# Optimization experiments

Measured on AMD Instinct MI355X. Metric: run time of the kernel, lower is better.

The kernel has to match this reference:

```python
import jax, jax.numpy as jnp
import numpy as np

ROPE_BASE = 10000.0

def _rope(x, positions):
    # x: [B, H, T, hs], rotate-half (GPT-NeoX style) rotary embedding
    hs = x.shape[-1]
    half = hs // 2
    inv_freq = 1.0 / (ROPE_BASE ** (jnp.arange(half, dtype=jnp.float32) / half))
    ang = positions.astype(jnp.float32)[:, None] * inv_freq[None, :]  # [T, half]
    cos, sin = jnp.cos(ang), jnp.sin(ang)
    x1, x2 = x[..., :half], x[..., half:]
    return jnp.concatenate([x1 * cos - x2 * sin, x1 * sin + x2 * cos], axis=-1)


def setup_inputs() -> dict:
    key = jax.random.key(0)
    ks = jax.random.split(key, 8)
    B, T, OFF, C, H = 1, 1024, 1024, 2048, 16
    hs = C // H
    return {
        "x": jax.random.normal(ks[0], (B, T, C), jnp.float32),
        "cached_k": jax.random.normal(ks[1], (B, H, OFF, hs), jnp.float32),
        "cached_v": jax.random.normal(ks[2], (B, H, OFF, hs), jnp.float32),
        "W_attn": jax.random.normal(ks[3], (C, 3 * C), jnp.float32) * 0.02,
        "b_attn": jnp.zeros((3 * C,), jnp.float32),
        "W_proj": jax.random.normal(ks[4], (C, C), jnp.float32) * 0.02,
        "b_proj": jnp.zeros((C,), jnp.float32),
        "decay_raw": jax.random.normal(ks[5], (16,), jnp.float32) * 0.5,
    }


def reference(x, cached_k, cached_v, W_attn, b_attn, W_proj, b_proj, decay_raw):
    B, T, C = x.shape
    H = decay_raw.shape[0]
    hs = C // H
    off = cached_k.shape[2]

    qkv = x @ W_attn + b_attn                       # [B, T, 3C]
    q, k, v = jnp.split(qkv, 3, axis=-1)
    to_heads = lambda t: t.reshape(B, T, H, hs).transpose(0, 2, 1, 3)  # [B,H,T,hs]
    q, k, v = to_heads(q), to_heads(k), to_heads(v)

    positions = jnp.arange(off, off + T)
    q = _rope(q, positions)
    k = _rope(k, positions)

    k = jnp.concatenate([cached_k, k], axis=2)      # [B, H, T_full, hs]
    v = jnp.concatenate([cached_v, v], axis=2)
    T_full = k.shape[2]

    # causal mask over full key length, offset for cache
    neg_inf = jnp.finfo(jnp.float32).min
    q_idx = positions                               # [T]
    k_idx = jnp.arange(T_full)                      # [T_full]
    causal = jnp.where(k_idx[None, :] > q_idx[:, None], neg_inf, 0.0)  # [T, T_full]

    # per-head distance-decay log-bias
    decay = jax.nn.softplus(decay_raw)              # [H]
    dist = jnp.maximum(q_idx[:, None] - k_idx[None, :], 0).astype(jnp.float32)
    logw = -jnp.log1p(decay[:, None, None] * jnp.log1p(dist))          # [H, T, T_full]
    bias = causal[None, :, :] + logw                # [H, T, T_full]

    scale = 1.0 / jnp.sqrt(jnp.float32(hs))
    scores = jnp.einsum('bhtd,bhsd->bhts', q, k) * scale + bias[None]
    attn = jax.nn.softmax(scores, axis=-1)
    y = jnp.einsum('bhts,bhsd->bhtd', attn, v)      # [B, H, T, hs]
    y = y.transpose(0, 2, 1, 3).reshape(B, T, C)
    y = y @ W_proj + b_proj
    return (y, k, v)
```

## Files before the change

kernel.cpp:

```cpp
#include <hip/hip_runtime.h>
#include <hip/hip_bf16.h>

typedef unsigned short u16;
typedef unsigned int u32;
typedef __attribute__((ext_vector_type(4))) float f32x4;
typedef __attribute__((ext_vector_type(8))) short bf16x8;

__device__ __forceinline__ u16 f2bf(float f) {
    union { float f; u32 u; } v; v.f = f;
    return (u16)((v.u + 0x7FFFu + ((v.u >> 16) & 1u)) >> 16);
}
__device__ __forceinline__ float bf2f(u16 b) {
    union { u32 u; float f; } v; v.u = ((u32)b) << 16;
    return v.f;
}
__device__ __forceinline__ void st_out(float* p, float v) { *p = v; }
__device__ __forceinline__ void st_out(u16* p, float v) { *p = f2bf(v); }

__device__ __forceinline__ f32x4 mfma16(bf16x8 a, bf16x8 b, f32x4 c) {
    return __builtin_amdgcn_mfma_f32_16x16x32_bf16(a, b, c, 0, 0, 0);
}

#define GLD_LDS16(g, l) __builtin_amdgcn_global_load_lds( \
    (const __attribute__((address_space(1))) void*)(g),   \
    (__attribute__((address_space(3))) void*)(l), 16, 0, 0)

__global__ __launch_bounds__(256) void k_prep(
    const float* __restrict__ W_attn, const float* __restrict__ W_proj,
    const float* __restrict__ x, const float* __restrict__ decay_raw,
    u16* __restrict__ WaT, u16* __restrict__ WpT, u16* __restrict__ Xb,
    float* __restrict__ bias_tab, float* __restrict__ cosT, float* __restrict__ sinT) {
    __shared__ float tile[64][65];
    const int b = blockIdx.x, tid = threadIdx.x;
    if (b < 4096) {
        const float* src; u16* dst; int R, Cc, bx, by;
        if (b < 3072) { src = W_attn; dst = WaT; R = 2048; Cc = 6144; bx = b % 96; by = b / 96; }
        else          { src = W_proj; dst = WpT; R = 2048; Cc = 2048; bx = (b - 3072) & 31; by = (b - 3072) >> 5; }
        int c0 = bx * 64, r0 = by * 64;
#pragma unroll
        for (int it = 0; it < 16; ++it) {
            int idx = it * 256 + tid;
            int r = idx >> 6, c = idx & 63;
            tile[r][c] = src[(size_t)(r0 + r) * Cc + c0 + c];
        }
        __syncthreads();
#pragma unroll
        for (int it = 0; it < 16; ++it) {
            int idx = it * 256 + tid;
            int cc = idx >> 6, rr = idx & 63;
            dst[(size_t)(c0 + cc) * R + r0 + rr] = f2bf(tile[rr][cc]);
        }
    } else if (b < 6144) {
        int i = (b - 4096) * 256 + tid;
        float4 v = ((const float4*)x)[i];
        u32 p0 = (u32)f2bf(v.x) | ((u32)f2bf(v.y) << 16);
        u32 p1 = (u32)f2bf(v.z) | ((u32)f2bf(v.w) << 16);
        uint2 p; p.x = p0; p.y = p1;
        *(uint2*)(Xb + (size_t)i * 4) = p;
    } else {
        int i = (b - 6144) * 256 + tid;
        if (i < 16 * 2048) {
            int h = i >> 11, dist = i & 2047;
            float dec = log1pf(expf(decay_raw[h]));
            bias_tab[i] = -log1pf(dec * log1pf((float)dist));
        }
        if (i < 1024 * 64) {
            int t = i >> 6, j = i & 63;
            float inv = expf(-logf(10000.0f) * (float)j / 64.0f);
            float ang = (float)(1024 + t) * inv;
            cosT[i] = cosf(ang);
            sinT[i] = sinf(ang);
        }
    }
}

template<int BM, int BN, int WRG, int WCG, typename OT>
__global__ __launch_bounds__(256) void k_gemm_bt(
    const u16* __restrict__ A, const u16* __restrict__ Bt,
    const float* __restrict__ bias, OT* __restrict__ C,
    int M, int N, int K) {
    constexpr int BK = 64;
    constexpr int WM = BM / WRG;
    constexpr int WN = BN / WCG;
    constexpr int MR = WM / 16;
    constexpr int NR = WN / 16;
    __shared__ char lds[(BM + BN) * BK * 2];
    char* ldsA = lds;
    char* ldsB = lds + BM * BK * 2;

    const int tid = threadIdx.x;
    const int lane = tid & 63, wid = tid >> 6;
    const int wr = wid / WCG, wc = wid % WCG;
    const int lhi = lane >> 4, llo = lane & 15;
    const int m0 = blockIdx.y * BM, n0 = blockIdx.x * BN;

    f32x4 acc[MR][NR];
#pragma unroll
    for (int m = 0; m < MR; ++m)
#pragma unroll
        for (int n = 0; n < NR; ++n)
            acc[m][n] = f32x4{0.f, 0.f, 0.f, 0.f};

    for (int k0 = 0; k0 < K; k0 += BK) {
#pragma unroll
        for (int it = 0; it < (BM * 8) / 256; ++it) {
            int ci = it * 256 + wid * 64 + lane;
            int r = ci >> 3, c = ci & 7;
            int sc = c ^ (r & 7);
            GLD_LDS16(A + (size_t)(m0 + r) * K + k0 + sc * 8,
                      ldsA + (it * 256 + wid * 64) * 16);
        }
#pragma unroll
        for (int it = 0; it < (BN * 8) / 256; ++it) {
            int ci = it * 256 + wid * 64 + lane;
            int r = ci >> 3, c = ci & 7;
            int sc = c ^ (r & 7);
            GLD_LDS16(Bt + (size_t)(n0 + r) * K + k0 + sc * 8,
                      ldsB + (it * 256 + wid * 64) * 16);
        }
        __syncthreads();
#pragma unroll
        for (int kk = 0; kk < BK; kk += 32) {
            bf16x8 af[MR], bfr[NR];
            const int clb = (kk >> 3) + lhi;
#pragma unroll
            for (int m = 0; m < MR; ++m) {
                int row = wr * WM + m * 16 + llo;
                af[m] = *(const bf16x8*)(ldsA + row * 128 + ((clb ^ (row & 7)) << 4));
            }
#pragma unroll
            for (int n = 0; n < NR; ++n) {
                int row = wc * WN + n * 16 + llo;
                bfr[n] = *(const bf16x8*)(ldsB + row * 128 + ((clb ^ (row & 7)) << 4));
            }
#pragma unroll
            for (int m = 0; m < MR; ++m)
#pragma unroll
                for (int n = 0; n < NR; ++n)
                    acc[m][n] = mfma16(af[m], bfr[n], acc[m][n]);
        }
        __syncthreads();
    }
#pragma unroll
    for (int m = 0; m < MR; ++m) {
        int row = m0 + wr * WM + m * 16 + lhi * 4;
#pragma unroll
        for (int n = 0; n < NR; ++n) {
            int col = n0 + wc * WN + n * 16 + llo;
            float bv = bias[col];
#pragma unroll
            for (int j = 0; j < 4; ++j)
                st_out(&C[(size_t)(row + j) * N + col], acc[m][n][j] + bv);
        }
    }
}

__global__ void k_fuse2(const u16* __restrict__ qkv,
                        const float* __restrict__ cosT, const float* __restrict__ sinT,
                        const float* __restrict__ cached_k,
                        u16* __restrict__ qb, u16* __restrict__ kb,
                        float* __restrict__ out_k) {
    const int b = blockIdx.x;
    if (b < 4096) {
        int i = b * 256 + threadIdx.x;
        int j = i & 63;
        int t = (i >> 6) & 1023;
        int h = i >> 16;
        const u16* row = qkv + (size_t)t * 6144;
        float q1 = bf2f(row[h * 128 + j]),        q2 = bf2f(row[h * 128 + j + 64]);
        float k1 = bf2f(row[2048 + h * 128 + j]), k2 = bf2f(row[2048 + h * 128 + j + 64]);
        float cv = cosT[t * 64 + j], sv = sinT[t * 64 + j];
        float qo1 = q1 * cv - q2 * sv, qo2 = q1 * sv + q2 * cv;
        float ko1 = k1 * cv - k2 * sv, ko2 = k1 * sv + k2 * cv;
        size_t qoff = ((size_t)h * 1024 + t) * 128 + j;
        qb[qoff] = f2bf(qo1); qb[qoff + 64] = f2bf(qo2);
        size_t koff = ((size_t)h * 2048 + 1024 + t) * 128 + j;
        kb[koff] = f2bf(ko1); kb[koff + 64] = f2bf(ko2);
        out_k[koff] = ko1; out_k[koff + 64] = ko2;
    } else {
        int i = (b - 4096) * 256 + threadIdx.x;
        int d = i & 127, s = (i >> 7) & 1023, h = i >> 17;
        float v = cached_k[i];
        size_t off = ((size_t)h * 2048 + s) * 128 + d;
        out_k[off] = v;
        kb[off] = f2bf(v);
    }
}

__global__ __launch_bounds__(256) void k_v_assemble(
    const float* __restrict__ cached_v, const u16* __restrict__ qkv,
    float* __restrict__ out_v, u16* __restrict__ vt) {
    __shared__ u16 tile[64][65];
    int s0 = blockIdx.x * 64, d0 = blockIdx.y * 64, h = blockIdx.z;
    int tid = threadIdx.x;
#pragma unroll
    for (int it = 0; it < 16; ++it) {
        int idx = it * 256 + tid;
        int r = idx >> 6, c = idx & 63;
        int s = s0 + r, d = d0 + c;
        u16 v = (s < 1024)
            ? f2bf(cached_v[((size_t)h * 1024 + s) * 128 + d])
            : qkv[(size_t)(s - 1024) * 6144 + 4096 + h * 128 + d];
        tile[r][c] = v;
        out_v[((size_t)h * 2048 + s) * 128 + d] = bf2f(v);
    }
    __syncthreads();
#pragma unroll
    for (int it = 0; it < 16; ++it) {
        int idx = it * 256 + tid;
        int dd = idx >> 6, ss = idx & 63;
        vt[((size_t)h * 128 + d0 + dd) * 2048 + s0 + ss] = tile[ss][dd];
    }
}

__global__ __launch_bounds__(256, 4) void k_attn(
    const u16* __restrict__ qb,
    const u16* __restrict__ kb,
    const u16* __restrict__ vt,
    const float* __restrict__ bias_tab,
    u16* __restrict__ Pacc,
    float* __restrict__ Pm,
    float* __restrict__ Pl) {
    __shared__ char ldsK[2][32 * 256];
    __shared__ char ldsV[2][128 * 64];
    __shared__ u16 ldsP[4][16 * 36];

    const int bid = blockIdx.x;
    const int xcd = bid & 7, idx = bid >> 3;
    const int work = xcd * 128 + idx;
    const int h = work >> 6, rem = work & 63;
    const int qt = rem >> 2, chunk = rem & 3;
    const int qbase = qt * 64;
    const int tid = threadIdx.x, lane = tid & 63, wid = tid >> 6;
    const int lhi = lane >> 4, llo = lane & 15;
    const int slot = (h * 16 + qt) * 4 + chunk;

    const u16* kg = kb + (size_t)h * 2048 * 128;
    const u16* vg = vt + (size_t)h * 128 * 2048;
    const float* bt = bias_tab + h * 2048;

    bf16x8 qf[4];
    {
        const u16* qrow = qb + ((size_t)h * 1024 + qbase + wid * 16 + llo) * 128;
#pragma unroll
        for (int c = 0; c < 4; ++c)
            qf[c] = *(const bf16x8*)(qrow + c * 32 + lhi * 8);
    }

    f32x4 acc[8];
#pragma unroll
    for (int d = 0; d < 8; ++d) acc[d] = f32x4{0.f, 0.f, 0.f, 0.f};
    float mrow[4] = {-3e38f, -3e38f, -3e38f, -3e38f};
    float lrow[4] = {0.f, 0.f, 0.f, 0.f};

    const int ntiles = 34 + 2 * qt;
    const float scale = 0.08838834764831845f;
    const int qpos = 1024 + qbase + wid * 16 + lhi * 4;

    auto stage = [&](int b, int st) {
        int sbase = st * 32;
#pragma unroll
        for (int it = 0; it < 2; ++it) {
            int ci = it * 256 + tid;
            int r = ci >> 4, c = ci & 15;
            int sc = c ^ (r & 7);
            GLD_LDS16(kg + (size_t)(sbase + r) * 128 + sc * 8,
                      &ldsK[b][0] + (it * 256 + wid * 64) * 16);
        }
#pragma unroll
        for (int it = 0; it < 2; ++it) {
            int ci = it * 256 + tid;
            int r = ci >> 2, c = ci & 3;
            int sc = c ^ ((r >> 1) & 3);
            GLD_LDS16(vg + (size_t)r * 2048 + sbase + sc * 8,
                      &ldsV[b][0] + (it * 256 + wid * 64) * 16);
        }
    };

    const int st0 = chunk + 4 * ((ntiles - 1 - chunk) >> 2);
    stage(0, st0);
    __syncthreads();
    int cur = 0;
    for (int st = st0; st >= chunk; st -= 4) {
        if (st >= chunk + 4) stage(cur ^ 1, st - 4);
        const int sbase = st * 32;
        const char* lK = &ldsK[cur][0];
        const char* lV = &ldsV[cur][0];

        f32x4 sc4[2];
#pragma unroll
        for (int sub = 0; sub < 2; ++sub) {
            f32x4 s4 = f32x4{0.f, 0.f, 0.f, 0.f};
            int key = sub * 16 + llo;
#pragma unroll
            for (int c2 = 0; c2 < 4; ++c2) {
                int cl = c2 * 4 + lhi;
                bf16x8 kf = *(const bf16x8*)(lK + key * 256 + ((cl ^ (key & 7)) << 4));
                s4 = mfma16(qf[c2], kf, s4);
            }
            sc4[sub] = s4;
        }

#pragma unroll
        for (int sub = 0; sub < 2; ++sub) {
            int key = sbase + sub * 16 + llo;
#pragma unroll
            for (int j = 0; j < 4; ++j) {
                int dist = qpos + j - key;
                float bv = bt[dist < 0 ? 0 : dist];
                sc4[sub][j] = (dist < 0) ? -3e38f : sc4[sub][j] * scale + bv;
            }
        }
        float tmax[4];
        int ok = 1;
#pragma unroll
        for (int j = 0; j < 4; ++j) {
            tmax[j] = fmaxf(sc4[0][j], sc4[1][j]);
            ok &= (tmax[j] <= mrow[j] + 8.0f) ? 1 : 0;
        }
        if (!__all(ok)) {
#pragma unroll
            for (int j = 0; j < 4; ++j) {
                float t = tmax[j];
                t = fmaxf(t, __shfl_xor(t, 1));
                t = fmaxf(t, __shfl_xor(t, 2));
                t = fmaxf(t, __shfl_xor(t, 4));
                t = fmaxf(t, __shfl_xor(t, 8));
                float mnew = fmaxf(mrow[j], t);
                float fs = __expf(mrow[j] - mnew);
                mrow[j] = mnew;
                lrow[j] *= fs;
#pragma unroll
                for (int d = 0; d < 8; ++d) acc[d][j] *= fs;
            }
        }
#pragma unroll
        for (int sub = 0; sub < 2; ++sub)
#pragma unroll
            for (int j = 0; j < 4; ++j) {
                float p = __expf(sc4[sub][j] - mrow[j]);
                sc4[sub][j] = p;
                lrow[j] += p;
            }

        u16* P = &ldsP[wid][0];
#pragma unroll
        for (int sub = 0; sub < 2; ++sub)
#pragma unroll
            for (int j = 0; j < 4; ++j)
                P[(lhi * 4 + j) * 36 + sub * 16 + llo] = f2bf(sc4[sub][j]);

        bf16x8 pf = *(const bf16x8*)((const char*)P + llo * 72 + lhi * 16);
#pragma unroll
        for (int db = 0; db < 8; ++db) {
            int dr = db * 16 + llo;
            int cl = lhi ^ ((dr >> 1) & 3);
            bf16x8 vf = *(const bf16x8*)(lV + dr * 64 + cl * 16);
            acc[db] = mfma16(pf, vf, acc[db]);
        }
        __syncthreads();
        cur ^= 1;
    }

#pragma unroll
    for (int j = 0; j < 4; ++j) {
        float t = lrow[j];
        t += __shfl_xor(t, 1);
        t += __shfl_xor(t, 2);
        t += __shfl_xor(t, 4);
        t += __shfl_xor(t, 8);
        lrow[j] = t;
    }

    if (llo == 0) {
#pragma unroll
        for (int j = 0; j < 4; ++j) {
            int r = wid * 16 + lhi * 4 + j;
            Pm[(size_t)slot * 64 + r] = mrow[j];
            Pl[(size_t)slot * 64 + r] = lrow[j];
        }
    }
#pragma unroll
    for (int db = 0; db < 8; ++db)
#pragma unroll
        for (int j = 0; j < 4; ++j) {
            int r = wid * 16 + lhi * 4 + j;
            Pacc[(size_t)slot * 8192 + r * 128 + db * 16 + llo] = f2bf(acc[db][j]);
        }
}

__global__ __launch_bounds__(256) void k_merge(
    const u16* __restrict__ Pacc, const float* __restrict__ Pm,
    const float* __restrict__ Pl, u16* __restrict__ yb) {
    const int h = blockIdx.x >> 4, qt = blockIdx.x & 15;
    const int slot0 = blockIdx.x * 4;
    const int tid = threadIdx.x;
    const int r = tid >> 2, d0 = (tid & 3) * 32;

    float m[4], l[4];
#pragma unroll
    for (int c = 0; c < 4; ++c) {
        m[c] = Pm[(size_t)(slot0 + c) * 64 + r];
        l[c] = Pl[(size_t)(slot0 + c) * 64 + r];
    }
    float M = fmaxf(fmaxf(m[0], m[1]), fmaxf(m[2], m[3]));
    float w[4], L = 0.f;
#pragma unroll
    for (int c = 0; c < 4; ++c) {
        w[c] = __expf(m[c] - M);
        L += w[c] * l[c];
    }
    float inv = 1.0f / L;

    float y[32];
#pragma unroll
    for (int i = 0; i < 32; ++i) y[i] = 0.f;
#pragma unroll
    for (int c = 0; c < 4; ++c) {
        const uint4* pa = (const uint4*)(Pacc + (size_t)(slot0 + c) * 8192 + r * 128 + d0);
        float wc = w[c];
#pragma unroll
        for (int q = 0; q < 4; ++q) {
            uint4 v = pa[q];
            u32 a[4] = {v.x, v.y, v.z, v.w};
#pragma unroll
            for (int p = 0; p < 4; ++p) {
                y[q * 8 + p * 2]     += wc * bf2f((u16)(a[p] & 0xFFFF));
                y[q * 8 + p * 2 + 1] += wc * bf2f((u16)(a[p] >> 16));
            }
        }
    }
    int trow = qt * 64 + r;
    uint4 outv[4];
    u32* ow = (u32*)outv;
#pragma unroll
    for (int k = 0; k < 16; ++k)
        ow[k] = (u32)f2bf(y[2 * k] * inv) | ((u32)f2bf(y[2 * k + 1] * inv) << 16);
    uint4* dst = (uint4*)(yb + (size_t)trow * 2048 + h * 128 + d0);
#pragma unroll
    for (int q = 0; q < 4; ++q) dst[q] = outv[q];
}

extern "C" void kernel_launch(void* const* d_in, const int* in_sizes, int n_in,
                              void* d_out, int out_size, void* d_ws, size_t ws_size,
                              hipStream_t stream) {
    (void)in_sizes; (void)n_in; (void)out_size;
    const float* x         = (const float*)d_in[0];
    const float* cached_k  = (const float*)d_in[1];
    const float* cached_v  = (const float*)d_in[2];
    const float* W_attn    = (const float*)d_in[3];
    const float* b_attn    = (const float*)d_in[4];
    const float* W_proj    = (const float*)d_in[5];
    const float* b_proj    = (const float*)d_in[6];
    const float* decay_raw = (const float*)d_in[7];

    float* out_y = (float*)d_out;
    float* out_k = out_y + 2097152;
    float* out_v = out_y + 6291456;

    char* ws = (char*)d_ws;
    if (ws_size < 63569920) return;
    u16*   WaT  = (u16*)(ws);
    u16*   WpT  = (u16*)(ws + 25165824);
    u16*   Xb   = (u16*)(ws + 33554432);
    u16*   QKVb = (u16*)(ws + 37748736);
    float* BT   = (float*)(ws + 62914560);
    float* CT   = (float*)(ws + 63045632);
    float* ST   = (float*)(ws + 63307776);
    u16*   Qb   = (u16*)(ws);
    u16*   Kb   = (u16*)(ws + 4194304);
    u16*   Vt   = (u16*)(ws + 12582912);
    u16*   Yb   = (u16*)(ws + 20971520);
    float* Pm   = (float*)(ws + 33554432);
    float* Pl   = (float*)(ws + 33816576);
    u16*   Pacc = (u16*)(ws + 37748736);

    k_prep<<<6400, 256, 0, stream>>>(W_attn, W_proj, x, decay_raw, WaT, WpT, Xb, BT, CT, ST);
    k_gemm_bt<128, 96, 2, 2, u16><<<dim3(64, 8), 256, 0, stream>>>(Xb, WaT, b_attn, QKVb, 1024, 6144, 2048);
    k_fuse2<<<12288, 256, 0, stream>>>(QKVb, CT, ST, cached_k, Qb, Kb, out_k);
    k_v_assemble<<<dim3(32, 2, 16), 256, 0, stream>>>(cached_v, QKVb, out_v, Vt);
    k_attn<<<1024, 256, 0, stream>>>(Qb, Kb, Vt, BT, Pacc, Pm, Pl);
    k_merge<<<256, 256, 0, stream>>>(Pacc, Pm, Pl, Yb);
    k_gemm_bt<64, 64, 2, 2, float><<<dim3(32, 16), 256, 0, stream>>>(Yb, WpT, b_proj, out_y, 1024, 2048, 2048);
}
```

Before: 145.2 us.

## Double-buffer GEMM LDS tiles, add MFMA priority hints, split merge across more blocks

The GEMM kernel now double-buffers its LDS tiles, so the global-to-LDS load of the next K tile is issued while the current tile is being multiplied. The QKV GEMM tile shrinks from 128x96 to 128x64, which launches more blocks and offsets the doubled LDS footprint. The attention kernel wraps its MFMA sections in s_setprio so matrix work from one wave is favoured over other waves. The merge kernel splits each head/query tile across four blocks, each handling a quarter of the head dimension, giving four times the blocks with fewer registers per thread. The costs are extra LDS per block, possibly lower occupancy, and redundant m/l reads in the merge.

```diff
diff --git a/kernel.cpp b/kernel.cpp
--- a/kernel.cpp
+++ b/kernel.cpp
@@ -84,9 +84,8 @@
     constexpr int WN = BN / WCG;
     constexpr int MR = WM / 16;
     constexpr int NR = WN / 16;
-    __shared__ char lds[(BM + BN) * BK * 2];
-    char* ldsA = lds;
-    char* ldsB = lds + BM * BK * 2;
+    constexpr int LDSZ = (BM + BN) * BK * 2;
+    __shared__ char lds[2][LDSZ];
 
     const int tid = threadIdx.x;
     const int lane = tid & 63, wid = tid >> 6;
@@ -101,7 +100,9 @@
         for (int n = 0; n < NR; ++n)
             acc[m][n] = f32x4{0.f, 0.f, 0.f, 0.f};
 
-    for (int k0 = 0; k0 < K; k0 += BK) {
+    auto stage = [&](int buf, int k0) {
+        char* ldsA = &lds[buf][0];
+        char* ldsB = &lds[buf][0] + BM * BK * 2;
 #pragma unroll
         for (int it = 0; it < (BM * 8) / 256; ++it) {
             int ci = it * 256 + wid * 64 + lane;
@@ -118,7 +119,15 @@
             GLD_LDS16(Bt + (size_t)(n0 + r) * K + k0 + sc * 8,
                       ldsB + (it * 256 + wid * 64) * 16);
         }
-        __syncthreads();
+    };
+
+    stage(0, 0);
+    __syncthreads();
+    int cur = 0;
+    for (int k0 = 0; k0 < K; k0 += BK) {
+        if (k0 + BK < K) stage(cur ^ 1, k0 + BK);
+        const char* ldsA = &lds[cur][0];
+        const char* ldsB = &lds[cur][0] + BM * BK * 2;
 #pragma unroll
         for (int kk = 0; kk < BK; kk += 32) {
             bf16x8 af[MR], bfr[NR];
@@ -140,6 +149,7 @@
                     acc[m][n] = mfma16(af[m], bfr[n], acc[m][n]);
         }
         __syncthreads();
+        cur ^= 1;
     }
 #pragma unroll
     for (int m = 0; m < MR; ++m) {
@@ -288,6 +298,7 @@
         const char* lV = &ldsV[cur][0];
 
         f32x4 sc4[2];
+        __builtin_amdgcn_s_setprio(1);
 #pragma unroll
         for (int sub = 0; sub < 2; ++sub) {
             f32x4 s4 = f32x4{0.f, 0.f, 0.f, 0.f};
@@ -300,6 +311,7 @@
             }
             sc4[sub] = s4;
         }
+        __builtin_amdgcn_s_setprio(0);
 
 #pragma unroll
         for (int sub = 0; sub < 2; ++sub) {
@@ -351,6 +363,7 @@
                 P[(lhi * 4 + j) * 36 + sub * 16 + llo] = f2bf(sc4[sub][j]);
 
         bf16x8 pf = *(const bf16x8*)((const char*)P + llo * 72 + lhi * 16);
+        __builtin_amdgcn_s_setprio(1);
 #pragma unroll
         for (int db = 0; db < 8; ++db) {
             int dr = db * 16 + llo;
@@ -358,6 +371,7 @@
             bf16x8 vf = *(const bf16x8*)(lV + dr * 64 + cl * 16);
             acc[db] = mfma16(pf, vf, acc[db]);
         }
+        __builtin_amdgcn_s_setprio(0);
         __syncthreads();
         cur ^= 1;
     }
@@ -392,10 +406,11 @@
 __global__ __launch_bounds__(256) void k_merge(
     const u16* __restrict__ Pacc, const float* __restrict__ Pm,
     const float* __restrict__ Pl, u16* __restrict__ yb) {
-    const int h = blockIdx.x >> 4, qt = blockIdx.x & 15;
-    const int slot0 = blockIdx.x * 4;
+    const int b = blockIdx.x;
+    const int h = b >> 6, qt = (b >> 2) & 15, quarter = b & 3;
+    const int slot0 = (h * 16 + qt) * 4;
     const int tid = threadIdx.x;
-    const int r = tid >> 2, d0 = (tid & 3) * 32;
+    const int r = tid >> 2, dd = (tid & 3) * 8 + quarter * 32;
 
     float m[4], l[4];
 #pragma unroll
@@ -412,33 +427,28 @@
     }
     float inv = 1.0f / L;
 
-    float y[32];
-#pragma unroll
-    for (int i = 0; i < 32; ++i) y[i] = 0.f;
+    float y[8];
+#pragma unroll
+    for (int i = 0; i < 8; ++i) y[i] = 0.f;
 #pragma unroll
     for (int c = 0; c < 4; ++c) {
-        const uint4* pa = (const uint4*)(Pacc + (size_t)(slot0 + c) * 8192 + r * 128 + d0);
+        const uint4* pa = (const uint4*)(Pacc + (size_t)(slot0 + c) * 8192 + r * 128 + dd);
         float wc = w[c];
-#pragma unroll
-        for (int q = 0; q < 4; ++q) {
-            uint4 v = pa[q];
-            u32 a[4] = {v.x, v.y, v.z, v.w};
-#pragma unroll
-            for (int p = 0; p < 4; ++p) {
-                y[q * 8 + p * 2]     += wc * bf2f((u16)(a[p] & 0xFFFF));
-                y[q * 8 + p * 2 + 1] += wc * bf2f((u16)(a[p] >> 16));
-            }
+        uint4 v = *pa;
+        u32 a[4] = {v.x, v.y, v.z, v.w};
+#pragma unroll
+        for (int p = 0; p < 4; ++p) {
+            y[p * 2]     += wc * bf2f((u16)(a[p] & 0xFFFF));
+            y[p * 2 + 1] += wc * bf2f((u16)(a[p] >> 16));
         }
     }
     int trow = qt * 64 + r;
-    uint4 outv[4];
-    u32* ow = (u32*)outv;
-#pragma unroll
-    for (int k = 0; k < 16; ++k)
+    uint4 outv;
+    u32* ow = (u32*)&outv;
+#pragma unroll
+    for (int k = 0; k < 4; ++k)
         ow[k] = (u32)f2bf(y[2 * k] * inv) | ((u32)f2bf(y[2 * k + 1] * inv) << 16);
-    uint4* dst = (uint4*)(yb + (size_t)trow * 2048 + h * 128 + d0);
-#pragma unroll
-    for (int q = 0; q < 4; ++q) dst[q] = outv[q];
+    *(uint4*)(yb + (size_t)trow * 2048 + h * 128 + dd) = outv;
 }
 
 extern "C" void kernel_launch(void* const* d_in, const int* in_sizes, int n_in,
@@ -476,10 +486,10 @@
     u16*   Pacc = (u16*)(ws + 37748736);
 
     k_prep<<<6400, 256, 0, stream>>>(W_attn, W_proj, x, decay_raw, WaT, WpT, Xb, BT, CT, ST);
-    k_gemm_bt<128, 96, 2, 2, u16><<<dim3(64, 8), 256, 0, stream>>>(Xb, WaT, b_attn, QKVb, 1024, 6144, 2048);
+    k_gemm_bt<128, 64, 2, 2, u16><<<dim3(96, 8), 256, 0, stream>>>(Xb, WaT, b_attn, QKVb, 1024, 6144, 2048);
     k_fuse2<<<12288, 256, 0, stream>>>(QKVb, CT, ST, cached_k, Qb, Kb, out_k);
     k_v_assemble<<<dim3(32, 2, 16), 256, 0, stream>>>(cached_v, QKVb, out_v, Vt);
     k_attn<<<1024, 256, 0, stream>>>(Qb, Kb, Vt, BT, Pacc, Pm, Pl);
-    k_merge<<<256, 256, 0, stream>>>(Pacc, Pm, Pl, Yb);
+    k_merge<<<1024, 256, 0, stream>>>(Pacc, Pm, Pl, Yb);
     k_gemm_bt<64, 64, 2, 2, float><<<dim3(32, 16), 256, 0, stream>>>(Yb, WpT, b_proj, out_y, 1024, 2048, 2048);
 }
```

Result: faster. 139.4 us (-4.0%).
